# Optimization experiments

Measured on AMD Instinct MI355X. Metric: run time of the kernel, lower is better.

Reference implementation:

```python
import jax, jax.numpy as jnp
import numpy as np
import math

D_MODEL = 1024
N_HEAD = 16
D_HEAD = D_MODEL // N_HEAD
INIT_SIZE = 1200  # RelativeSinusoidalPositionalEmbedding init_size
SCALE = 1.0       # scale=False in __init__


def _rel_pos_embed(L, d_head):
    """Replicates RelativeSinusoidalPositionalEmbedding: table over positions
    [-601, 600] (num=init_size+1=1201 rows), padding row 0 zeroed, then gather
    rows for positions arange(-L/2, L/2) + origin_shift (origin_shift=601)."""
    num = INIT_SIZE + 1                      # 1201
    half = d_head // 2
    freq = jnp.exp(jnp.arange(half, dtype=jnp.float32) * (-math.log(10000.0) / (half - 1)))
    pos_vals = jnp.arange(-num // 2, num // 2, dtype=jnp.float32)   # -601..599 -> 1201 vals
    ang = pos_vals[:, None] * freq[None, :]
    table = jnp.concatenate([jnp.sin(ang), jnp.cos(ang)], axis=1)   # [num, d_head]
    table = table.at[0].set(0.0)             # padding_idx = 0
    origin_shift = num // 2 + 1              # 601
    idx = jnp.arange(-(L // 2), L // 2) + origin_shift   # L even -> L indices
    return table[idx]                        # [L, d_head]


def setup_inputs() -> dict:
    key = jax.random.key(0)
    k1, k2, k3, k4, k5 = jax.random.split(key, 5)
    B, L = 4, 1024
    embed = jax.random.normal(k1, (B, L, D_MODEL), dtype=jnp.float32)
    umask = jnp.ones((B, L), dtype=jnp.int32)                       # 1 = valid utterance
    qmask = jax.random.randint(k2, (B, L), 0, 2).astype(jnp.int64)  # speaker ids {0,1}
    W_qkv = jax.random.normal(k3, (D_MODEL, 4 * D_MODEL), dtype=jnp.float32) * 0.02
    W_pos = jax.random.normal(k4, (D_HEAD, 3 * D_MODEL), dtype=jnp.float32) * 0.02
    W_fc  = jax.random.normal(k5, (D_MODEL, D_MODEL), dtype=jnp.float32) * 0.02
    return {"embed": embed, "umask": umask, "qmask": qmask,
            "W_qkv": W_qkv, "W_pos": W_pos, "W_fc": W_fc}


def reference(embed, umask, qmask, W_qkv, W_pos, W_fc):
    B, L, d = embed.shape
    H, dh = N_HEAD, d // N_HEAD

    # qkv projection and head split
    q, k1, k2, v = jnp.split(embed @ W_qkv, 4, axis=-1)             # each [B, L, d]
    q  = q.reshape(B, L, H, dh).transpose(0, 2, 1, 3)               # [B, H, L, dh]
    k1 = k1.reshape(B, L, H, dh).transpose(0, 2, 1, 3)
    k2 = k2.reshape(B, L, H, dh).transpose(0, 2, 1, 3)
    v  = v.reshape(B, L, H, dh).transpose(0, 2, 1, 3)

    # relative position projections (detached sinusoids -> qk_pos linear)
    pe = _rel_pos_embed(L, dh)                                      # [L, dh]
    qp, kp1, kp2 = jnp.split(pe @ W_pos, 3, axis=-1)                # each [L, d]
    qp  = qp.reshape(L, H, dh).transpose(1, 0, 2)                   # [H, L, dh]
    kp1 = kp1.reshape(L, H, dh).transpose(1, 0, 2)
    kp2 = kp2.reshape(L, H, dh).transpose(1, 0, 2)

    pos1 = jnp.einsum('hqd,hkd->hqk', qp, kp1)                      # [H, L, L]
    pos2 = jnp.einsum('hqd,hkd->hqk', qp, kp2)

    attn_self  = jnp.einsum('bhqd,bhkd->bhqk', q, k1) + pos1[None]  # [B, H, L, L]
    attn_other = jnp.einsum('bhqd,bhkd->bhqk', q, k2) + pos2[None]

    # same-speaker mask: self-attn only where speakers match, other-attn where they differ
    qeq = (qmask[:, :, None] == qmask[:, None, :])                  # [B, L, L] bool
    attn_self  = jnp.where(qeq[:, None], attn_self, 0.0)
    attn_other = jnp.where(qeq[:, None], 0.0, attn_other)
    attn_add = (attn_self + attn_other) / SCALE

    # causal (order) mask + padding mask (eval-mode path of the module)
    order = jnp.triu(jnp.ones((L, L), dtype=bool), 1)[None] | (umask == 0)[:, None, :]
    attn = jnp.where(order[:, None], -jnp.inf, attn_add)
    p = jax.nn.softmax(attn, axis=-1)                               # dropout is identity in eval

    out = jnp.einsum('bhqk,bhkd->bhqd', p, v)                       # [B, H, L, dh]
    out = out.transpose(0, 2, 1, 3).reshape(B, L, d)
    return out @ W_fc
```

## Files before the change

kernel.cpp:

```cpp
#include <hip/hip_runtime.h>
#include <math.h>

#define NB 4
#define SEQ 1024
#define DMODEL 1024
#define NHEAD 16
#define DHEAD 64

typedef __attribute__((ext_vector_type(8))) short s16x8;
typedef __attribute__((ext_vector_type(4))) short s16x4;
typedef __attribute__((ext_vector_type(4))) float f32x4;

__device__ __forceinline__ short f2bf(float f) {
    union { float f; unsigned u; } x; x.f = f;
    unsigned r = x.u + 0x7fffu + ((x.u >> 16) & 1u);
    return (short)(r >> 16);
}

__device__ __forceinline__ unsigned cvtpk(float lo, float hi) {
    unsigned r;
    asm("v_cvt_pk_bf16_f32 %0, %1, %2" : "=v"(r) : "v"(lo), "v"(hi));
    return r;
}

__device__ __forceinline__ f32x4 mfma16(s16x8 a, s16x8 b, f32x4 c) {
    return __builtin_amdgcn_mfma_f32_16x16x32_bf16(a, b, c, 0, 0, 0);
}

__device__ __forceinline__ s16x8 cvt8(float4 a, float4 b) {
    s16x8 v;
    v[0] = f2bf(a.x); v[1] = f2bf(a.y); v[2] = f2bf(a.z); v[3] = f2bf(a.w);
    v[4] = f2bf(b.x); v[5] = f2bf(b.y); v[6] = f2bf(b.z); v[7] = f2bf(b.w);
    return v;
}

__device__ __forceinline__ s16x8 ldlds(const short* base, int byteoff) {
    return *(const s16x8*)((const char*)base + byteoff);
}

#define GLDS16(g, l) __builtin_amdgcn_global_load_lds( \
    (const __attribute__((address_space(1))) unsigned int*)(g), \
    (__attribute__((address_space(3))) unsigned int*)(l), 16, 0, 0)
#define GLDS4(g, l) __builtin_amdgcn_global_load_lds( \
    (const __attribute__((address_space(1))) unsigned int*)(g), \
    (__attribute__((address_space(3))) unsigned int*)(l), 4, 0, 0)

__global__ __launch_bounds__(256) void prep_a_kernel(
    const float* __restrict__ embed, const float* __restrict__ Wqkv,
    short* __restrict__ ebf, short* __restrict__ WqkvT)
{
    __shared__ __align__(16) char smem[9216];
    int gb = blockIdx.x;
    int tid = threadIdx.x;

    if (gb < 2048) {
        int i = (gb * 256 + tid) * 8;
        float4 a = *(const float4*)(embed + i);
        float4 b = *(const float4*)(embed + i + 4);
        *(s16x8*)(ebf + i) = cvt8(a, b);
    } else {
        int t = gb - 2048;
        int bx = t & 63, by = t >> 6;
        const int N = 4096;
        short (*T)[72] = (short(*)[72])smem;
        int nt = bx * 64, kt = by * 64;
        int kl = tid >> 4;
        int nl = (tid & 15) * 4;
        #pragma unroll
        for (int rr = 0; rr < 4; ++rr) {
            int k = kl + rr * 16;
            float4 v = *(const float4*)(Wqkv + (size_t)(kt + k) * N + nt + nl);
            T[nl + 0][k] = f2bf(v.x);
            T[nl + 1][k] = f2bf(v.y);
            T[nl + 2][k] = f2bf(v.z);
            T[nl + 3][k] = f2bf(v.w);
        }
        __syncthreads();
        int nr = tid >> 2;
        int kc = (tid & 3) * 16;
        uint4 a = *(const uint4*)&T[nr][kc];
        uint4 b = *(const uint4*)&T[nr][kc + 8];
        short* dst = WqkvT + (size_t)(nt + nr) * 1024 + kt + kc;
        *(uint4*)(dst) = a;
        *(uint4*)(dst + 8) = b;
    }
}

__global__ __launch_bounds__(512, 2) void gemm_qkv_fused(
    const short* __restrict__ A, const short* __restrict__ BT,
    short* __restrict__ o0, short* __restrict__ o1, short* __restrict__ o2,
    short* __restrict__ o3,
    const int* __restrict__ qmask, const int* __restrict__ umask,
    const float* __restrict__ Wpos, const float* __restrict__ Wfc,
    int* __restrict__ PM, short* __restrict__ qpb, short* __restrict__ WfcT)
{
    __shared__ short As[2][256 * 32];
    __shared__ short Bs[2][256 * 32];

    int gb = blockIdx.x;
    int tid = threadIdx.x;

    if (gb >= 256) {
        int pb = gb - 256;
        char* smem = (char*)&As[0][0];
        if (pb < 4) {
            if (tid < 256) {
                int b = pb;
                for (int k = tid; k < 1088; k += 256) {
                    int v = 2;
                    if (k < 1024)
                        v = (qmask[b * 1024 + k] & 1) | ((umask[b * 1024 + k] == 0) ? 2 : 0);
                    PM[b * 1088 + k] = v;
                }
            }
        } else if (pb < 388) {
            int bid = pb - 4;
            int s = bid >> 7;
            int l0 = (bid & 127) * 8;
            float (*pe)[64] = (float(*)[64])smem;

            if (tid < 256) {
                for (int idx = tid; idx < 512; idx += 256) {
                    int li = idx >> 6, t = idx & 63;
                    float p = (float)(l0 + li - 512);
                    int j = (t < 32) ? t : (t - 32);
                    float f = expf(-0.2971077539f * (float)j);
                    float a = p * f;
                    pe[li][t] = (t < 32) ? sinf(a) : cosf(a);
                }
            }
            __syncthreads();

            if (tid < 256) {
                float acc[4][8] = {};
                const float* wp = Wpos + s * 1024 + tid;
                for (int t = 0; t < 64; ++t) {
                    float w0 = wp[t * 3072];
                    float w1 = wp[t * 3072 + 256];
                    float w2 = wp[t * 3072 + 512];
                    float w3 = wp[t * 3072 + 768];
                    #pragma unroll
                    for (int li = 0; li < 8; ++li) {
                        float pv = pe[li][t];
                        acc[0][li] += pv * w0; acc[1][li] += pv * w1;
                        acc[2][li] += pv * w2; acc[3][li] += pv * w3;
                    }
                }
                #pragma unroll
                for (int cc = 0; cc < 4; ++cc) {
                    int c = tid + cc * 256;
                    int h = c >> 6, d = c & 63;
                    #pragma unroll
                    for (int li = 0; li < 8; ++li) {
                        short bv = f2bf(acc[cc][li]);
                        if (s == 0) {
                            qpb[((size_t)(h << 10) + l0 + li) * 64 + d] = bv;
                        } else {
                            short* dst = (s == 1) ? o1 : o2;
                            #pragma unroll
                            for (int bb = 0; bb < 4; ++bb)
                                dst[((size_t)((bb * 16 + h) * 1024) + l0 + li) * 128 + 64 + d] = bv;
                        }
                    }
                }
            }
        } else {
            int t = pb - 388;
            int bx = t & 15, by = t >> 4;
            const int N = 1024;
            short (*T)[72] = (short(*)[72])smem;
            int nt = bx * 64, kt = by * 64;
            if (tid < 256) {
                int kl = tid >> 4;
                int nl = (tid & 15) * 4;
                #pragma unroll
                for (int rr = 0; rr < 4; ++rr) {
                    int k = kl + rr * 16;
                    float4 v = *(const float4*)(Wfc + (size_t)(kt + k) * N + nt + nl);
                    T[nl + 0][k] = f2bf(v.x);
                    T[nl + 1][k] = f2bf(v.y);
                    T[nl + 2][k] = f2bf(v.z);
                    T[nl + 3][k] = f2bf(v.w);
                }
            }
            __syncthreads();
            if (tid < 256) {
                int nr = tid >> 2;
                int kc = (tid & 3) * 16;
                uint4 a = *(const uint4*)&T[nr][kc];
                uint4 b = *(const uint4*)&T[nr][kc + 8];
                short* dst = WfcT + (size_t)(nt + nr) * 1024 + kt + kc;
                *(uint4*)(dst) = a;
                *(uint4*)(dst + 8) = b;
            }
        }
        return;
    }

    int lin = gb;
    int swb = (lin & 7) * 32 + (lin >> 3);
    int bx = swb & 15, by = swb >> 4;
    int m0 = by * 256, n0 = bx * 256;

    int w = tid >> 6, lane = tid & 63;
    int wm = w >> 2, wn = w & 3;
    int lq = lane & 15, lg = lane >> 4;

    f32x4 zero = {0.f, 0.f, 0.f, 0.f};
    f32x4 acc[8][4];
    #pragma unroll
    for (int i = 0; i < 8; ++i)
        #pragma unroll
        for (int jj = 0; jj < 4; ++jj) acc[i][jj] = zero;

    int swz = (((lane & 3) ^ ((lane >> 2) & 3)) << 3);
    int srow = lane >> 2;
    const short* aBase = A  + (size_t)(m0 + (w << 5) + srow) * 1024 + swz;
    const short* bBase = BT + (size_t)(n0 + (w << 5) + srow) * 1024 + swz;
    int dOff = w * 1024;

    GLDS16(aBase, &As[0][dOff]);
    GLDS16(aBase + 16 * 1024, &As[0][dOff + 512]);
    GLDS16(bBase, &Bs[0][dOff]);
    GLDS16(bBase + 16 * 1024, &Bs[0][dOff + 512]);

    int cur = 0;
    for (int kt = 0; kt < 1024; kt += 32) {
        if (kt + 32 < 1024) {
            int nxt = cur ^ 1;
            GLDS16(aBase + kt + 32, &As[nxt][dOff]);
            GLDS16(aBase + kt + 32 + 16 * 1024, &As[nxt][dOff + 512]);
            GLDS16(bBase + kt + 32, &Bs[nxt][dOff]);
            GLDS16(bBase + kt + 32 + 16 * 1024, &Bs[nxt][dOff + 512]);
            asm volatile("s_waitcnt vmcnt(4)" ::: "memory");
        } else {
            asm volatile("s_waitcnt vmcnt(0)" ::: "memory");
        }
        __builtin_amdgcn_s_barrier();
        asm volatile("" ::: "memory");

        s16x8 bfr[4];
        #pragma unroll
        for (int nt = 0; nt < 4; ++nt) {
            int row = wn * 64 + nt * 16 + lq;
            bfr[nt] = ldlds(Bs[cur], (row * 64 + lg * 16) ^ ((row & 3) << 4));
        }
        #pragma unroll
        for (int mt = 0; mt < 8; ++mt) {
            int row = wm * 128 + mt * 16 + lq;
            s16x8 af = ldlds(As[cur], (row * 64 + lg * 16) ^ ((row & 3) << 4));
            #pragma unroll
            for (int nt = 0; nt < 4; ++nt)
                acc[mt][nt] = mfma16(af, bfr[nt], acc[mt][nt]);
        }

        asm volatile("" ::: "memory");
        __builtin_amdgcn_s_barrier();
        cur ^= 1;
    }

    #pragma unroll
    for (int nt = 0; nt < 4; ++nt) {
        int n = n0 + wn * 64 + nt * 16 + lq;
        int sec = n >> 10, hd = n & 1023;
        int hh = hd >> 6, d = hd & 63;
        #pragma unroll
        for (int mt = 0; mt < 8; ++mt) {
            int mb = m0 + wm * 128 + mt * 16 + lg * 4;
            int b = mb >> 10, li0 = mb & 1023;
            int bh = b * 16 + hh;
            if (sec == 3) {
                s16x4 pv;
                #pragma unroll
                for (int r = 0; r < 4; ++r) pv[r] = f2bf(acc[mt][nt][r]);
                *(s16x4*)(o3 + (((size_t)(bh * 64 + d)) << 10) + li0) = pv;
            } else {
                #pragma unroll
                for (int r = 0; r < 4; ++r) {
                    short bv = f2bf(acc[mt][nt][r]);
                    if (sec == 0)
                        o0[((size_t)(bh << 10) + li0 + r) * 64 + d] = bv;
                    else if (sec == 1)
                        o1[((size_t)bh * 1024 + li0 + r) * 128 + d] = bv;
                    else
                        o2[((size_t)bh * 1024 + li0 + r) * 128 + d] = bv;
                }
            }
        }
    }
}

template<int EPI, int NCOLS>
__global__ __launch_bounds__(256) void gemm_nt(
    const short* __restrict__ A, const short* __restrict__ BT,
    float* __restrict__ of)
{
    __shared__ short As[2][128 * 32];
    __shared__ short Bs[2][128 * 32];

    int nwg = gridDim.x * gridDim.y;
    int lin = blockIdx.y * gridDim.x + blockIdx.x;
    int cpx = nwg >> 3;
    int swb = (lin & 7) * cpx + (lin >> 3);
    int bx = swb % gridDim.x, by = swb / gridDim.x;
    int m0 = by * 128, n0 = bx * 128;

    int tid = threadIdx.x;
    int w = tid >> 6, lane = tid & 63;
    int wm = w >> 1, wn = w & 1;
    int lq = lane & 15, lg = lane >> 4;

    f32x4 zero = {0.f, 0.f, 0.f, 0.f};
    f32x4 acc[4][4];
    #pragma unroll
    for (int i = 0; i < 4; ++i)
        #pragma unroll
        for (int j = 0; j < 4; ++j) acc[i][j] = zero;

    int swz = (((lane & 3) ^ ((lane >> 2) & 3)) << 3);
    int srow = lane >> 2;
    const short* aBase = A  + (size_t)(m0 + (w << 5) + srow) * 1024 + swz;
    const short* bBase = BT + (size_t)(n0 + (w << 5) + srow) * 1024 + swz;
    int dOff = w * 1024;

    GLDS16(aBase, &As[0][dOff]);
    GLDS16(aBase + 16 * 1024, &As[0][dOff + 512]);
    GLDS16(bBase, &Bs[0][dOff]);
    GLDS16(bBase + 16 * 1024, &Bs[0][dOff + 512]);

    int cur = 0;
    for (int kt = 0; kt < 1024; kt += 32) {
        if (kt + 32 < 1024) {
            int nxt = cur ^ 1;
            GLDS16(aBase + kt + 32, &As[nxt][dOff]);
            GLDS16(aBase + kt + 32 + 16 * 1024, &As[nxt][dOff + 512]);
            GLDS16(bBase + kt + 32, &Bs[nxt][dOff]);
            GLDS16(bBase + kt + 32 + 16 * 1024, &Bs[nxt][dOff + 512]);
            asm volatile("s_waitcnt vmcnt(4)" ::: "memory");
        } else {
            asm volatile("s_waitcnt vmcnt(0)" ::: "memory");
        }
        __builtin_amdgcn_s_barrier();
        asm volatile("" ::: "memory");

        s16x8 af[4], bfr[4];
        #pragma unroll
        for (int mt = 0; mt < 4; ++mt) {
            int row = wm * 64 + mt * 16 + lq;
            af[mt] = ldlds(As[cur], (row * 64 + lg * 16) ^ ((row & 3) << 4));
        }
        #pragma unroll
        for (int nt = 0; nt < 4; ++nt) {
            int row = wn * 64 + nt * 16 + lq;
            bfr[nt] = ldlds(Bs[cur], (row * 64 + lg * 16) ^ ((row & 3) << 4));
        }
        #pragma unroll
        for (int mt = 0; mt < 4; ++mt)
            #pragma unroll
            for (int nt = 0; nt < 4; ++nt)
                acc[mt][nt] = mfma16(af[mt], bfr[nt], acc[mt][nt]);

        asm volatile("" ::: "memory");
        __builtin_amdgcn_s_barrier();
        cur ^= 1;
    }

    #pragma unroll
    for (int nt = 0; nt < 4; ++nt) {
        int n = n0 + wn * 64 + nt * 16 + lq;
        #pragma unroll
        for (int mt = 0; mt < 4; ++mt) {
            int mb = m0 + wm * 64 + mt * 16 + lg * 4;
            #pragma unroll
            for (int r = 0; r < 4; ++r)
                of[(size_t)(mb + r) * NCOLS + n] = acc[mt][nt][r];
        }
    }
}

__global__ __launch_bounds__(256) void attn_kernel(
    const short* __restrict__ qb, const short* __restrict__ k1cat,
    const short* __restrict__ k2cat, const short* __restrict__ vtb,
    const short* __restrict__ qpb, const int* __restrict__ PM,
    const int* __restrict__ qmask, short* __restrict__ ctx)
{
    __shared__ short K1s[2][32 * 128];
    __shared__ short K2s[2][32 * 128];
    __shared__ short Vs[64 * 32];
    __shared__ int   PMs[2][64];

    int bid = blockIdx.x;
    int xg = bid & 7, j = bid >> 3;
    int bh = xg * 8 + (j & 7);
    int qt = 15 - (j >> 3);
    int b = bh >> 4, h = bh & 15;

    int w = threadIdx.x >> 6, lane = threadIdx.x & 63;
    int lq = lane & 15, lg = lane >> 4;

    auto STAGE_K = [&](int d, int K0) {
        #pragma unroll
        for (int i = 0; i < 4; ++i) {
            int g = w * 4 + i;
            if (g < 8) {
                int row = g * 4 + (lane >> 4);
                int colb = ((lane & 15) << 4) ^ ((row & 7) << 4);
                const short* src = k1cat + ((size_t)bh * 1024 + K0 + row) * 128 + (colb >> 1);
                GLDS16(src, &K1s[d][g * 512]);
            } else {
                int gg = g - 8;
                int row = gg * 4 + (lane >> 4);
                int colb = ((lane & 15) << 4) ^ ((row & 7) << 4);
                const short* src = k2cat + ((size_t)bh * 1024 + K0 + row) * 128 + (colb >> 1);
                GLDS16(src, &K2s[d][gg * 512]);
            }
        }
        if (w == 0) {
            GLDS4(PM + b * 1088 + K0 + lane, &PMs[d][0]);
        }
    };
    auto STAGE_V = [&](int K0) {
        int row = w * 16 + (lane >> 2);
        int colb = ((lane & 3) << 4) ^ ((row & 3) << 4);
        const short* src = vtb + ((size_t)bh * 64 + row) * 1024 + K0 + (colb >> 1);
        GLDS16(src, &Vs[w * 512]);
    };

    f32x4 zero = {0.f, 0.f, 0.f, 0.f};

    int q0 = qt * 64 + w * 16;
    int q_glob = q0 + lq;

    const short* qrow  = qb  + ((size_t)bh * SEQ + q_glob) * DHEAD;
    const short* qprow = qpb + ((size_t)h  * SEQ + q_glob) * DHEAD;
    s16x8 qf0  = *(const s16x8*)(qrow + lg * 8);
    s16x8 qf1  = *(const s16x8*)(qrow + 32 + lg * 8);
    s16x8 qpf0 = *(const s16x8*)(qprow + lg * 8);
    s16x8 qpf1 = *(const s16x8*)(qprow + 32 + lg * 8);
    int qm_q = qmask[b * SEQ + q_glob] & 1;
    asm volatile("s_waitcnt vmcnt(0)" ::: "memory");

    f32x4 accO[4];
    #pragma unroll
    for (int i = 0; i < 4; ++i) accO[i] = zero;
    float m_run = -1e30f, l_run = 0.f;

    int nslab = 2 * qt + 2;
    STAGE_K(0, 0);
    STAGE_V(0);

    #pragma unroll 1
    for (int t = 0; t < nslab; ++t) {
        int cur = t & 1;
        if (t + 1 < nslab) {
            STAGE_K(cur ^ 1, (t + 1) * 32);
            if (w == 0) asm volatile("s_waitcnt vmcnt(5)" ::: "memory");
            else        asm volatile("s_waitcnt vmcnt(4)" ::: "memory");
        } else {
            asm volatile("s_waitcnt vmcnt(0)" ::: "memory");
        }
        __builtin_amdgcn_s_barrier();
        asm volatile("" ::: "memory");

        int K0 = t * 32;
        if (K0 <= q0 + 15) {
            const short* b1 = K1s[cur];
            const short* b2 = K2s[cur];

            f32x4 s1v[2], s2v[2];
            __builtin_amdgcn_s_setprio(1);
            #pragma unroll
            for (int hh = 0; hh < 2; ++hh) {
                int row = hh * 16 + lq;
                int ro = row * 256 + (lg << 4);
                int sw = (row & 7) << 4;
                f32x4 tv = zero, uv = zero;
                tv = mfma16(ldlds(b1, (ro      ) ^ sw), qf0,  tv);
                tv = mfma16(ldlds(b1, (ro +  64) ^ sw), qf1,  tv);
                tv = mfma16(ldlds(b1, (ro + 128) ^ sw), qpf0, tv);
                tv = mfma16(ldlds(b1, (ro + 192) ^ sw), qpf1, tv);
                s1v[hh] = tv;
                uv = mfma16(ldlds(b2, (ro      ) ^ sw), qf0,  uv);
                uv = mfma16(ldlds(b2, (ro +  64) ^ sw), qf1,  uv);
                uv = mfma16(ldlds(b2, (ro + 128) ^ sw), qpf0, uv);
                uv = mfma16(ldlds(b2, (ro + 192) ^ sw), qpf1, uv);
                s2v[hh] = uv;
            }
            __builtin_amdgcn_s_setprio(0);

            int4 pmv0 = *(const int4*)&PMs[cur][lg * 4];
            int4 pmv1 = *(const int4*)&PMs[cur][16 + lg * 4];
            int pme[8] = {pmv0.x, pmv0.y, pmv0.z, pmv0.w,
                          pmv1.x, pmv1.y, pmv1.z, pmv1.w};

            float sv[8];
            #pragma unroll
            for (int i = 0; i < 8; ++i) {
                int hh = i >> 2, r = i & 3;
                int k_idx = K0 + hh * 16 + lg * 4 + r;
                int pm = pme[i];
                float s = ((pm & 1) == qm_q) ? s1v[hh][r] : s2v[hh][r];
                if (k_idx > q_glob || (pm & 2)) s = -INFINITY;
                sv[i] = s;
            }
            float tm = sv[0];
            #pragma unroll
            for (int i = 1; i < 8; ++i) tm = fmaxf(tm, sv[i]);
            tm = fmaxf(tm, __shfl_xor(tm, 16));
            tm = fmaxf(tm, __shfl_xor(tm, 32));

            if (!__all(tm <= m_run + 8.0f)) {
                float m_new = fmaxf(m_run, tm);
                float scale = __expf(m_run - m_new);
                m_run = m_new;
                l_run *= scale;
                f32x4 scv;
                scv[0] = __shfl(scale, lg * 4 + 0);
                scv[1] = __shfl(scale, lg * 4 + 1);
                scv[2] = __shfl(scale, lg * 4 + 2);
                scv[3] = __shfl(scale, lg * 4 + 3);
                #pragma unroll
                for (int dt = 0; dt < 4; ++dt) accO[dt] *= scv;
            }

            float p[8]; float ps = 0.f;
            #pragma unroll
            for (int i = 0; i < 8; ++i) { p[i] = __expf(sv[i] - m_run); ps += p[i]; }
            ps += __shfl_xor(ps, 16);
            ps += __shfl_xor(ps, 32);
            l_run += ps;

            unsigned dA0 = cvtpk(p[0], p[1]);
            unsigned dA1 = cvtpk(p[2], p[3]);
            unsigned dB0 = cvtpk(p[4], p[5]);
            unsigned dB1 = cvtpk(p[6], p[7]);
            int sl0 = lq + ((lg & 1) << 5);
            int sl1 = sl0 + 16;
            unsigned a0 = (unsigned)__shfl((int)dA0, sl0), a1 = (unsigned)__shfl((int)dA1, sl0);
            unsigned a2 = (unsigned)__shfl((int)dA0, sl1), a3 = (unsigned)__shfl((int)dA1, sl1);
            unsigned c0 = (unsigned)__shfl((int)dB0, sl0), c1 = (unsigned)__shfl((int)dB1, sl0);
            unsigned c2 = (unsigned)__shfl((int)dB0, sl1), c3 = (unsigned)__shfl((int)dB1, sl1);
            bool hi = (lg >= 2);
            union { unsigned u[4]; s16x8 v; } pa;
            pa.u[0] = hi ? c0 : a0; pa.u[1] = hi ? c1 : a1;
            pa.u[2] = hi ? c2 : a2; pa.u[3] = hi ? c3 : a3;

            __builtin_amdgcn_s_setprio(1);
            #pragma unroll
            for (int dt = 0; dt < 4; ++dt) {
                int vrow = dt * 16 + lq;
                int voff = (vrow * 64 + (lg << 4)) ^ ((vrow & 3) << 4);
                accO[dt] = mfma16(pa.v, ldlds(Vs, voff), accO[dt]);
            }
            __builtin_amdgcn_s_setprio(0);
        }

        asm volatile("" ::: "memory");
        __builtin_amdgcn_s_barrier();
        if (t + 1 < nslab) STAGE_V((t + 1) * 32);
    }

    float inv = 1.0f / l_run;
    f32x4 invv;
    invv[0] = __shfl(inv, lg * 4 + 0);
    invv[1] = __shfl(inv, lg * 4 + 1);
    invv[2] = __shfl(inv, lg * 4 + 2);
    invv[3] = __shfl(inv, lg * 4 + 3);
    #pragma unroll
    for (int dt = 0; dt < 4; ++dt) {
        #pragma unroll
        for (int r = 0; r < 4; ++r) {
            int qo = q0 + lg * 4 + r;
            size_t off = ((size_t)(b * SEQ + qo)) * DMODEL + h * DHEAD + dt * 16 + lq;
            ctx[off] = f2bf(accO[dt][r] * invv[r]);
        }
    }
}

extern "C" void kernel_launch(void* const* d_in, const int* in_sizes, int n_in,
                              void* d_out, int out_size, void* d_ws, size_t ws_size,
                              hipStream_t stream) {
    const float* embed = (const float*)d_in[0];
    const int*   umask = (const int*)d_in[1];
    const int*   qmask = (const int*)d_in[2];
    const float* Wqkv  = (const float*)d_in[3];
    const float* Wpos  = (const float*)d_in[4];
    const float* Wfc   = (const float*)d_in[5];
    float* out = (float*)d_out;

    char* w = (char*)d_ws;
    short* qb    = (short*)(w + (0ull  << 20));
    short* vtb   = (short*)(w + (8ull  << 20));
    short* qpb   = (short*)(w + (16ull << 20));
    short* ctx   = (short*)(w + (18ull << 20));
    short* ebf   = ctx;
    short* k1cat = (short*)(w + (26ull << 20));
    short* k2cat = (short*)(w + (42ull << 20));
    int*   PM    = (int*)  (w + (58ull << 20));
    short* WqkvT = (short*)(w + (59ull << 20));
    short* WfcT  = (short*)(w + (67ull << 20));

    hipLaunchKernelGGL(prep_a_kernel, dim3(3072), dim3(256), 0, stream,
                       embed, Wqkv, ebf, WqkvT);
    hipLaunchKernelGGL(gemm_qkv_fused, dim3(900), dim3(512), 0, stream,
                       ebf, WqkvT, qb, k1cat, k2cat, vtb,
                       qmask, umask, Wpos, Wfc, PM, qpb, WfcT);
    hipLaunchKernelGGL(attn_kernel, dim3(1024), dim3(256), 0, stream,
                       qb, k1cat, k2cat, vtb, qpb, PM, qmask, ctx);
    hipLaunchKernelGGL((gemm_nt<1, 1024>), dim3(8, 32), dim3(256), 0, stream,
                       ctx, WfcT, out);
}
```

Measured before the change: 155.9 us.

## Move side prep work into prep kernel and deepen QKV GEMM pipeline to 4 stages

The positional-projection, mask packing and W_fc transpose blocks move out of the QKV GEMM kernel into the first prep kernel, so the GEMM launch holds only the 256 GEMM tiles. The GEMM's LDS staging grows from double-buffered to a 4-deep ring with three tiles prefetched ahead, and the vmcnt waits are adjusted to match. The aim is to hide global-load latency better and stop side work from competing with GEMM tiles. LDS use doubles to 128KB per block, which limits how many blocks fit per CU despite the launch_bounds(512,2) hint.

```diff
diff --git a/kernel.cpp b/kernel.cpp
--- a/kernel.cpp
+++ b/kernel.cpp
@@ -47,7 +47,12 @@
 
 __global__ __launch_bounds__(256) void prep_a_kernel(
     const float* __restrict__ embed, const float* __restrict__ Wqkv,
-    short* __restrict__ ebf, short* __restrict__ WqkvT)
+    const int* __restrict__ qmask, const int* __restrict__ umask,
+    const float* __restrict__ Wpos, const float* __restrict__ Wfc,
+    short* __restrict__ ebf, short* __restrict__ WqkvT,
+    int* __restrict__ PM, short* __restrict__ qpb,
+    short* __restrict__ k1cat, short* __restrict__ k2cat,
+    short* __restrict__ WfcT)
 {
     __shared__ __align__(16) char smem[9216];
     int gb = blockIdx.x;
@@ -58,7 +63,7 @@
         float4 a = *(const float4*)(embed + i);
         float4 b = *(const float4*)(embed + i + 4);
         *(s16x8*)(ebf + i) = cvt8(a, b);
-    } else {
+    } else if (gb < 3072) {
         int t = gb - 2048;
         int bx = t & 63, by = t >> 6;
         const int N = 4096;
@@ -83,125 +88,103 @@
         short* dst = WqkvT + (size_t)(nt + nr) * 1024 + kt + kc;
         *(uint4*)(dst) = a;
         *(uint4*)(dst + 8) = b;
-    }
-}
-
-__global__ __launch_bounds__(512, 2) void gemm_qkv_fused(
+    } else if (gb < 3076) {
+        int b = gb - 3072;
+        for (int k = tid; k < 1088; k += 256) {
+            int v = 2;
+            if (k < 1024)
+                v = (qmask[b * 1024 + k] & 1) | ((umask[b * 1024 + k] == 0) ? 2 : 0);
+            PM[b * 1088 + k] = v;
+        }
+    } else if (gb < 3460) {
+        int bid = gb - 3076;
+        int s = bid >> 7;
+        int l0 = (bid & 127) * 8;
+        float (*pe)[64] = (float(*)[64])smem;
+
+        for (int idx = tid; idx < 512; idx += 256) {
+            int li = idx >> 6, t = idx & 63;
+            float p = (float)(l0 + li - 512);
+            int j = (t < 32) ? t : (t - 32);
+            float f = expf(-0.2971077539f * (float)j);
+            float a = p * f;
+            pe[li][t] = (t < 32) ? sinf(a) : cosf(a);
+        }
+        __syncthreads();
+
+        float acc[4][8] = {};
+        const float* wp = Wpos + s * 1024 + tid;
+        for (int t = 0; t < 64; ++t) {
+            float w0 = wp[t * 3072];
+            float w1 = wp[t * 3072 + 256];
+            float w2 = wp[t * 3072 + 512];
+            float w3 = wp[t * 3072 + 768];
+            #pragma unroll
+            for (int li = 0; li < 8; ++li) {
+                float pv = pe[li][t];
+                acc[0][li] += pv * w0; acc[1][li] += pv * w1;
+                acc[2][li] += pv * w2; acc[3][li] += pv * w3;
+            }
+        }
+        #pragma unroll
+        for (int cc = 0; cc < 4; ++cc) {
+            int c = tid + cc * 256;
+            int h = c >> 6, d = c & 63;
+            #pragma unroll
+            for (int li = 0; li < 8; ++li) {
+                short bv = f2bf(acc[cc][li]);
+                if (s == 0) {
+                    qpb[((size_t)(h << 10) + l0 + li) * 64 + d] = bv;
+                } else {
+                    short* dst = (s == 1) ? k1cat : k2cat;
+                    #pragma unroll
+                    for (int bb = 0; bb < 4; ++bb)
+                        dst[((size_t)((bb * 16 + h) * 1024) + l0 + li) * 128 + 64 + d] = bv;
+                }
+            }
+        }
+    } else {
+        int t = gb - 3460;
+        int bx = t & 15, by = t >> 4;
+        const int N = 1024;
+        short (*T)[72] = (short(*)[72])smem;
+        int nt = bx * 64, kt = by * 64;
+        int kl = tid >> 4;
+        int nl = (tid & 15) * 4;
+        #pragma unroll
+        for (int rr = 0; rr < 4; ++rr) {
+            int k = kl + rr * 16;
+            float4 v = *(const float4*)(Wfc + (size_t)(kt + k) * N + nt + nl);
+            T[nl + 0][k] = f2bf(v.x);
+            T[nl + 1][k] = f2bf(v.y);
+            T[nl + 2][k] = f2bf(v.z);
+            T[nl + 3][k] = f2bf(v.w);
+        }
+        __syncthreads();
+        int nr = tid >> 2;
+        int kc = (tid & 3) * 16;
+        uint4 a = *(const uint4*)&T[nr][kc];
+        uint4 b = *(const uint4*)&T[nr][kc + 8];
+        short* dst = WfcT + (size_t)(nt + nr) * 1024 + kt + kc;
+        *(uint4*)(dst) = a;
+        *(uint4*)(dst + 8) = b;
+    }
+}
+
+__global__ __launch_bounds__(512, 2) void gemm_qkv(
     const short* __restrict__ A, const short* __restrict__ BT,
     short* __restrict__ o0, short* __restrict__ o1, short* __restrict__ o2,
-    short* __restrict__ o3,
-    const int* __restrict__ qmask, const int* __restrict__ umask,
-    const float* __restrict__ Wpos, const float* __restrict__ Wfc,
-    int* __restrict__ PM, short* __restrict__ qpb, short* __restrict__ WfcT)
+    short* __restrict__ o3)
 {
-    __shared__ short As[2][256 * 32];
-    __shared__ short Bs[2][256 * 32];
-
-    int gb = blockIdx.x;
-    int tid = threadIdx.x;
-
-    if (gb >= 256) {
-        int pb = gb - 256;
-        char* smem = (char*)&As[0][0];
-        if (pb < 4) {
-            if (tid < 256) {
-                int b = pb;
-                for (int k = tid; k < 1088; k += 256) {
-                    int v = 2;
-                    if (k < 1024)
-                        v = (qmask[b * 1024 + k] & 1) | ((umask[b * 1024 + k] == 0) ? 2 : 0);
-                    PM[b * 1088 + k] = v;
-                }
-            }
-        } else if (pb < 388) {
-            int bid = pb - 4;
-            int s = bid >> 7;
-            int l0 = (bid & 127) * 8;
-            float (*pe)[64] = (float(*)[64])smem;
-
-            if (tid < 256) {
-                for (int idx = tid; idx < 512; idx += 256) {
-                    int li = idx >> 6, t = idx & 63;
-                    float p = (float)(l0 + li - 512);
-                    int j = (t < 32) ? t : (t - 32);
-                    float f = expf(-0.2971077539f * (float)j);
-                    float a = p * f;
-                    pe[li][t] = (t < 32) ? sinf(a) : cosf(a);
-                }
-            }
-            __syncthreads();
-
-            if (tid < 256) {
-                float acc[4][8] = {};
-                const float* wp = Wpos + s * 1024 + tid;
-                for (int t = 0; t < 64; ++t) {
-                    float w0 = wp[t * 3072];
-                    float w1 = wp[t * 3072 + 256];
-                    float w2 = wp[t * 3072 + 512];
-                    float w3 = wp[t * 3072 + 768];
-                    #pragma unroll
-                    for (int li = 0; li < 8; ++li) {
-                        float pv = pe[li][t];
-                        acc[0][li] += pv * w0; acc[1][li] += pv * w1;
-                        acc[2][li] += pv * w2; acc[3][li] += pv * w3;
-                    }
-                }
-                #pragma unroll
-                for (int cc = 0; cc < 4; ++cc) {
-                    int c = tid + cc * 256;
-                    int h = c >> 6, d = c & 63;
-                    #pragma unroll
-                    for (int li = 0; li < 8; ++li) {
-                        short bv = f2bf(acc[cc][li]);
-                        if (s == 0) {
-                            qpb[((size_t)(h << 10) + l0 + li) * 64 + d] = bv;
-                        } else {
-                            short* dst = (s == 1) ? o1 : o2;
-                            #pragma unroll
-                            for (int bb = 0; bb < 4; ++bb)
-                                dst[((size_t)((bb * 16 + h) * 1024) + l0 + li) * 128 + 64 + d] = bv;
-                        }
-                    }
-                }
-            }
-        } else {
-            int t = pb - 388;
-            int bx = t & 15, by = t >> 4;
-            const int N = 1024;
-            short (*T)[72] = (short(*)[72])smem;
-            int nt = bx * 64, kt = by * 64;
-            if (tid < 256) {
-                int kl = tid >> 4;
-                int nl = (tid & 15) * 4;
-                #pragma unroll
-                for (int rr = 0; rr < 4; ++rr) {
-                    int k = kl + rr * 16;
-                    float4 v = *(const float4*)(Wfc + (size_t)(kt + k) * N + nt + nl);
-                    T[nl + 0][k] = f2bf(v.x);
-                    T[nl + 1][k] = f2bf(v.y);
-                    T[nl + 2][k] = f2bf(v.z);
-                    T[nl + 3][k] = f2bf(v.w);
-                }
-            }
-            __syncthreads();
-            if (tid < 256) {
-                int nr = tid >> 2;
-                int kc = (tid & 3) * 16;
-                uint4 a = *(const uint4*)&T[nr][kc];
-                uint4 b = *(const uint4*)&T[nr][kc + 8];
-                short* dst = WfcT + (size_t)(nt + nr) * 1024 + kt + kc;
-                *(uint4*)(dst) = a;
-                *(uint4*)(dst + 8) = b;
-            }
-        }
-        return;
-    }
-
-    int lin = gb;
+    __shared__ short As[4][256 * 32];
+    __shared__ short Bs[4][256 * 32];
+
+    int lin = blockIdx.x;
     int swb = (lin & 7) * 32 + (lin >> 3);
     int bx = swb & 15, by = swb >> 4;
     int m0 = by * 256, n0 = bx * 256;
 
+    int tid = threadIdx.x;
     int w = tid >> 6, lane = tid & 63;
     int wm = w >> 2, wn = w & 3;
     int lq = lane & 15, lg = lane >> 4;
@@ -219,19 +202,26 @@
     const short* bBase = BT + (size_t)(n0 + (w << 5) + srow) * 1024 + swz;
     int dOff = w * 1024;
 
-    GLDS16(aBase, &As[0][dOff]);
-    GLDS16(aBase + 16 * 1024, &As[0][dOff + 512]);
-    GLDS16(bBase, &Bs[0][dOff]);
-    GLDS16(bBase + 16 * 1024, &Bs[0][dOff + 512]);
-
-    int cur = 0;
+    #define STAGEG(D, KT) {                                       \
+        GLDS16(aBase + (KT), &As[D][dOff]);                       \
+        GLDS16(aBase + (KT) + 16 * 1024, &As[D][dOff + 512]);     \
+        GLDS16(bBase + (KT), &Bs[D][dOff]);                       \
+        GLDS16(bBase + (KT) + 16 * 1024, &Bs[D][dOff + 512]);     \
+    }
+
+    STAGEG(0, 0);
+    STAGEG(1, 32);
+    STAGEG(2, 64);
+
     for (int kt = 0; kt < 1024; kt += 32) {
-        if (kt + 32 < 1024) {
-            int nxt = cur ^ 1;
-            GLDS16(aBase + kt + 32, &As[nxt][dOff]);
-            GLDS16(aBase + kt + 32 + 16 * 1024, &As[nxt][dOff + 512]);
-            GLDS16(bBase + kt + 32, &Bs[nxt][dOff]);
-            GLDS16(bBase + kt + 32 + 16 * 1024, &Bs[nxt][dOff + 512]);
+        int t = kt >> 5;
+        int cur = t & 3;
+        if (kt + 96 < 1024) {
+            STAGEG((t + 3) & 3, kt + 96);
+            asm volatile("s_waitcnt vmcnt(12)" ::: "memory");
+        } else if (kt + 64 < 1024) {
+            asm volatile("s_waitcnt vmcnt(8)" ::: "memory");
+        } else if (kt + 32 < 1024) {
             asm volatile("s_waitcnt vmcnt(4)" ::: "memory");
         } else {
             asm volatile("s_waitcnt vmcnt(0)" ::: "memory");
@@ -256,8 +246,8 @@
 
         asm volatile("" ::: "memory");
         __builtin_amdgcn_s_barrier();
-        cur ^= 1;
-    }
+    }
+    #undef STAGEG
 
     #pragma unroll
     for (int nt = 0; nt < 4; ++nt) {
@@ -600,11 +590,11 @@
     short* WqkvT = (short*)(w + (59ull << 20));
     short* WfcT  = (short*)(w + (67ull << 20));
 
-    hipLaunchKernelGGL(prep_a_kernel, dim3(3072), dim3(256), 0, stream,
-                       embed, Wqkv, ebf, WqkvT);
-    hipLaunchKernelGGL(gemm_qkv_fused, dim3(900), dim3(512), 0, stream,
-                       ebf, WqkvT, qb, k1cat, k2cat, vtb,
-                       qmask, umask, Wpos, Wfc, PM, qpb, WfcT);
+    hipLaunchKernelGGL(prep_a_kernel, dim3(3716), dim3(256), 0, stream,
+                       embed, Wqkv, qmask, umask, Wpos, Wfc,
+                       ebf, WqkvT, PM, qpb, k1cat, k2cat, WfcT);
+    hipLaunchKernelGGL(gemm_qkv, dim3(256), dim3(512), 0, stream,
+                       ebf, WqkvT, qb, k1cat, k2cat, vtb);
     hipLaunchKernelGGL(attn_kernel, dim3(1024), dim3(256), 0, stream,
                        qb, k1cat, k2cat, vtb, qpb, PM, qmask, ctx);
     hipLaunchKernelGGL((gemm_nt<1, 1024>), dim3(8, 32), dim3(256), 0, stream,
```

New measurement: 161.4 us. 1.04x slower.
